# Kernel optimization log

Measured on AMD Instinct MI355X. Metric: run time of the kernel, lower is better.

Reference implementation:

```python
import jax, jax.numpy as jnp
import numpy as np
import math

B, N, M = 4, 2048, 2048
DIM_Q = DIM_K = DIM_V = 1024
H = 16

def setup_inputs() -> dict:
    key = jax.random.key(0)
    ks = jax.random.split(key, 10)
    s = 0.02
    return {
        "Q": jax.random.normal(ks[0], (B, N, DIM_Q), jnp.float32),
        "K": jax.random.normal(ks[1], (B, M, DIM_K), jnp.float32),
        "Wq": jax.random.normal(ks[2], (DIM_V, DIM_Q), jnp.float32) * s,
        "bq": jax.random.normal(ks[3], (DIM_V,), jnp.float32) * s,
        "Wk": jax.random.normal(ks[4], (DIM_V, DIM_K), jnp.float32) * s,
        "bk": jax.random.normal(ks[5], (DIM_V,), jnp.float32) * s,
        "Wv": jax.random.normal(ks[6], (DIM_V, DIM_K), jnp.float32) * s,
        "bv": jax.random.normal(ks[7], (DIM_V,), jnp.float32) * s,
        "Wo": jax.random.normal(ks[8], (DIM_V, DIM_V), jnp.float32) * s,
        "bo": jax.random.normal(ks[9], (DIM_V,), jnp.float32) * s,
    }

def reference(Q, K, Wq, bq, Wk, bk, Wv, bv, Wo, bo):
    d = DIM_V // H  # head dim
    Qp = Q @ Wq.T + bq            # [B,N,DIM_V]
    Kp = K @ Wk.T + bk            # [B,M,DIM_V]
    Vp = K @ Wv.T + bv            # [B,M,DIM_V]
    # split heads: [B,T,H,d] -> [B,H,T,d]
    Qh = Qp.reshape(B, N, H, d).transpose(0, 2, 1, 3)
    Kh = Kp.reshape(B, M, H, d).transpose(0, 2, 1, 3)
    Vh = Vp.reshape(B, M, H, d).transpose(0, 2, 1, 3)
    # NOTE: original scales by sqrt(dim_V), not sqrt(head_dim)
    scores = jnp.einsum('bhnd,bhmd->bhnm', Qh, Kh) / math.sqrt(DIM_V)
    A = jax.nn.softmax(scores, axis=-1)
    Oh = Qh + jnp.einsum('bhnm,bhmd->bhnd', A, Vh)   # residual with projected Q
    O = Oh.transpose(0, 2, 1, 3).reshape(B, N, DIM_V)
    O = O + jax.nn.relu(O @ Wo.T + bo)
    return O
```

## Files before the change

### kernel.cpp

```cpp
#include <hip/hip_runtime.h>
#include <cstddef>
#include <cstdint>


typedef unsigned short ushort_t;
typedef __attribute__((ext_vector_type(8))) short bf16x8;
typedef __attribute__((ext_vector_type(4))) float floatx4;
typedef __attribute__((ext_vector_type(2))) float f32x2;
typedef __attribute__((ext_vector_type(2))) __bf16 b16x2;
typedef __attribute__((ext_vector_type(4))) unsigned short us4;

__device__ __forceinline__ ushort_t f2bf(float x) {
  union { float f; unsigned u; } v; v.f = x;
  unsigned r = v.u + 0x7FFFu + ((v.u >> 16) & 1u);
  return (ushort_t)(r >> 16);
}
__device__ __forceinline__ float bf2f(ushort_t x) {
  union { unsigned u; float f; } v; v.u = ((unsigned)x) << 16;
  return v.f;
}
__device__ __forceinline__ unsigned pk2(float a, float b) {
  union { float f; unsigned u; } x, y; x.f = a; y.f = b;
  return __builtin_amdgcn_perm(y.u + 0x8000u, x.u + 0x8000u, 0x07060302u);
}
__device__ __forceinline__ unsigned pk2c(float a, float b) {
  union { b16x2 v; unsigned u; } r;
  r.v = __builtin_convertvector((f32x2){a, b}, b16x2);
  return r.u;
}
__device__ __forceinline__ floatx4 mfma16(bf16x8 a, bf16x8 b, floatx4 c) {
  return __builtin_amdgcn_mfma_f32_16x16x32_bf16(a, b, c, 0, 0, 0);
}
__device__ __forceinline__ void gld_lds16(const void* g, void* l) {
  __builtin_amdgcn_global_load_lds(
      (const __attribute__((address_space(1))) unsigned int*)g,
      (__attribute__((address_space(3))) unsigned int*)l, 16, 0, 0);
}

__global__ void cvt6(const float* __restrict__ i0, const float* __restrict__ i1,
                     const float* __restrict__ i2, const float* __restrict__ i3,
                     const float* __restrict__ i4, const float* __restrict__ i5,
                     ushort_t* __restrict__ o0, ushort_t* __restrict__ o1,
                     ushort_t* __restrict__ o2, ushort_t* __restrict__ o3,
                     ushort_t* __restrict__ o4, ushort_t* __restrict__ o5) {
  int z = blockIdx.z;
  const float* in = z == 0 ? i0 : z == 1 ? i1 : z == 2 ? i2 : z == 3 ? i3 : z == 4 ? i4 : i5;
  ushort_t* out = z == 0 ? o0 : z == 1 ? o1 : z == 2 ? o2 : z == 3 ? o3 : z == 4 ? o4 : o5;
  int n8 = (z < 2) ? 1048576 : 131072;
  int i = blockIdx.x * 256 + threadIdx.x;
  if (i < n8) {
    const float4* p = (const float4*)in + (size_t)i * 2;
    float4 a = p[0], b = p[1];
    uint4 o;
    o.x = pk2(a.x, a.y); o.y = pk2(a.z, a.w);
    o.z = pk2(b.x, b.y); o.w = pk2(b.z, b.w);
    *((uint4*)out + i) = o;
  }
}

__global__ __launch_bounds__(256, 2)
void gemm_qkv(const ushort_t* __restrict__ Qb, const ushort_t* __restrict__ Kb,
              const ushort_t* __restrict__ Wqb, const ushort_t* __restrict__ Wkb,
              const ushort_t* __restrict__ Wvb,
              const float* __restrict__ bq, const float* __restrict__ bk,
              const float* __restrict__ bv,
              ushort_t* __restrict__ Qp, ushort_t* __restrict__ Kp,
              ushort_t* __restrict__ Vt)
{
  const int Kd = 1024, Nn = 1024;
  const int z = blockIdx.z;
  const ushort_t* Ab = (z == 0) ? Qb : Kb;
  const ushort_t* Bw = (z == 0) ? Wqb : (z == 1) ? Wkb : Wvb;
  const float* bias  = (z == 0) ? bq : (z == 1) ? bk : bv;

  __shared__ __align__(16) ushort_t As[128][64];
  __shared__ __align__(16) ushort_t Bs[128][64];
  const int tid = threadIdx.x;
  const int lane = tid & 63, wave = tid >> 6;
  const int wm = (wave >> 1) * 64, wn = (wave & 1) * 64;
  const int rq = lane & 15, kg = lane >> 4;

  const int wg = blockIdx.x, xcd = wg & 7, slot = wg >> 3;
  const int by = xcd * 8 + (slot >> 3);
  const int bx = slot & 7;
  const int row0 = by * 128, col0 = bx * 128;

  const int st_sub = lane >> 3;
  const int st_cs  = (lane & 7) ^ st_sub;

  floatx4 acc[4][4];
#pragma unroll
  for (int i = 0; i < 4; ++i)
#pragma unroll
    for (int j = 0; j < 4; ++j) acc[i][j] = (floatx4){0.f, 0.f, 0.f, 0.f};

  for (int k0 = 0; k0 < Kd; k0 += 64) {
    __syncthreads();
#pragma unroll
    for (int r = 0; r < 4; ++r) {
      int i = wave * 4 + r;
      int row = i * 8 + st_sub;
      gld_lds16(Ab + (size_t)(row0 + row) * Kd + k0 + st_cs * 8, (ushort_t*)As + i * 512);
      gld_lds16(Bw + (size_t)(col0 + row) * Kd + k0 + st_cs * 8, (ushort_t*)Bs + i * 512);
    }
    __syncthreads();
#pragma unroll
    for (int kq = 0; kq < 2; ++kq) {
      bf16x8 af[4], bfr[4];
#pragma unroll
      for (int mi = 0; mi < 4; ++mi)
        af[mi] = *(const bf16x8*)&As[wm + mi*16 + rq][((kq*4 + kg) ^ (rq & 7)) * 8];
#pragma unroll
      for (int ni = 0; ni < 4; ++ni)
        bfr[ni] = *(const bf16x8*)&Bs[wn + ni*16 + rq][((kq*4 + kg) ^ (rq & 7)) * 8];
#pragma unroll
      for (int mi = 0; mi < 4; ++mi)
#pragma unroll
        for (int ni = 0; ni < 4; ++ni)
          acc[mi][ni] = mfma16(af[mi], bfr[ni], acc[mi][ni]);
    }
  }

  float bv4[4];
#pragma unroll
  for (int ni = 0; ni < 4; ++ni) bv4[ni] = bias[col0 + wn + ni*16 + rq];

  if (z < 2) {
    ushort_t* Cb = (z == 0) ? Qp : Kp;
#pragma unroll
    for (int mi = 0; mi < 4; ++mi)
#pragma unroll
      for (int ni = 0; ni < 4; ++ni)
#pragma unroll
        for (int rr = 0; rr < 4; ++rr) {
          int row = row0 + wm + mi*16 + kg*4 + rr;
          int col = col0 + wn + ni*16 + rq;
          Cb[(size_t)row * Nn + col] = f2bf(acc[mi][ni][rr] + bv4[ni]);
        }
  } else {
#pragma unroll
    for (int mi = 0; mi < 4; ++mi)
#pragma unroll
      for (int ni = 0; ni < 4; ++ni) {
        int col = col0 + wn + ni*16 + rq;
        int base32 = row0 + wm + (mi >> 1) * 32;
        int p = kg * 8 + (mi & 1) * 4;
        us4 o = { f2bf(acc[mi][ni][0] + bv4[ni]), f2bf(acc[mi][ni][1] + bv4[ni]),
                  f2bf(acc[mi][ni][2] + bv4[ni]), f2bf(acc[mi][ni][3] + bv4[ni]) };
        *(us4*)(Vt + (size_t)col * 8192 + base32 + p) = o;
      }
  }
}

__global__ __launch_bounds__(256, 2)
void gemm_out(const ushort_t* __restrict__ Ob, const ushort_t* __restrict__ Bw,
              const float* __restrict__ bias, float* __restrict__ Out)
{
  const int Kd = 1024, Nn = 1024;
  __shared__ __align__(16) ushort_t As[128][64];
  __shared__ __align__(16) ushort_t Bs[128][64];
  const int tid = threadIdx.x;
  const int lane = tid & 63, wave = tid >> 6;
  const int wm = (wave >> 1) * 64, wn = (wave & 1) * 64;
  const int rq = lane & 15, kg = lane >> 4;

  const int wg = blockIdx.x, xcd = wg & 7, slot = wg >> 3;
  const int by = xcd * 8 + (slot >> 3);
  const int bx = slot & 7;
  const int row0 = by * 128, col0 = bx * 128;

  const int st_sub = lane >> 3;
  const int st_cs  = (lane & 7) ^ st_sub;

  floatx4 acc[4][4];
#pragma unroll
  for (int i = 0; i < 4; ++i)
#pragma unroll
    for (int j = 0; j < 4; ++j) acc[i][j] = (floatx4){0.f, 0.f, 0.f, 0.f};

  for (int k0 = 0; k0 < Kd; k0 += 64) {
    __syncthreads();
#pragma unroll
    for (int r = 0; r < 4; ++r) {
      int i = wave * 4 + r;
      int row = i * 8 + st_sub;
      gld_lds16(Ob + (size_t)(row0 + row) * Kd + k0 + st_cs * 8, (ushort_t*)As + i * 512);
      gld_lds16(Bw + (size_t)(col0 + row) * Kd + k0 + st_cs * 8, (ushort_t*)Bs + i * 512);
    }
    __syncthreads();
#pragma unroll
    for (int kq = 0; kq < 2; ++kq) {
      bf16x8 af[4], bfr[4];
#pragma unroll
      for (int mi = 0; mi < 4; ++mi)
        af[mi] = *(const bf16x8*)&As[wm + mi*16 + rq][((kq*4 + kg) ^ (rq & 7)) * 8];
#pragma unroll
      for (int ni = 0; ni < 4; ++ni)
        bfr[ni] = *(const bf16x8*)&Bs[wn + ni*16 + rq][((kq*4 + kg) ^ (rq & 7)) * 8];
#pragma unroll
      for (int mi = 0; mi < 4; ++mi)
#pragma unroll
        for (int ni = 0; ni < 4; ++ni)
          acc[mi][ni] = mfma16(af[mi], bfr[ni], acc[mi][ni]);
    }
  }

  float bv4[4];
#pragma unroll
  for (int ni = 0; ni < 4; ++ni) bv4[ni] = bias[col0 + wn + ni*16 + rq];
#pragma unroll
  for (int mi = 0; mi < 4; ++mi)
#pragma unroll
    for (int ni = 0; ni < 4; ++ni)
#pragma unroll
      for (int rr = 0; rr < 4; ++rr) {
        int row = row0 + wm + mi*16 + kg*4 + rr;
        int col = col0 + wn + ni*16 + rq;
        size_t idx = (size_t)row * Nn + col;
        float pre = acc[mi][ni][rr] + bv4[ni];
        Out[idx] = bf2f(Ob[idx]) + (pre > 0.f ? pre : 0.f);
      }
}

__global__ __launch_bounds__(256, 2)
void attn_kernel(const ushort_t* __restrict__ Qp,
                 const ushort_t* __restrict__ Kp,
                 const ushort_t* __restrict__ Vt,
                 ushort_t* __restrict__ Ob)
{
  const float sc2 = 0.045084439f;
  const int wg = blockIdx.x, xcd = wg & 7, slot = wg >> 3;
  const int bh = xcd * 8 + (slot >> 4);
  const int qt = slot & 15;
  const int b = bh >> 4, h = bh & 15;
  const int q0 = qt * 128;

  __shared__ __align__(16) ushort_t Ks[2][8192];
  __shared__ __align__(16) ushort_t Vs[2][8192];

  const int tid = threadIdx.x, lane = tid & 63, wq = tid >> 6;
  const int rq = lane & 15, kg = lane >> 4;

  const size_t qkbase = (size_t)(b * 2048) * 1024 + h * 64;

  const int sg_sub = lane >> 3;
  const int sg_csk = (lane & 7) ^ sg_sub;

#pragma unroll
  for (int r = 0; r < 4; ++r) {
    int i = wq * 4 + r;
    int row = i * 8 + sg_sub;
    gld_lds16(Qp + qkbase + (size_t)(q0 + row) * 1024 + sg_csk * 8, &Ks[1][i * 512]);
  }
  __syncthreads();

  auto stage = [&](int kt, int bufi) {
    const int kv0 = kt * 128;
#pragma unroll
    for (int r = 0; r < 4; ++r) {
      int i = wq * 4 + r;
      int rowk = i * 8 + sg_sub;
      gld_lds16(Kp + qkbase + (size_t)(kv0 + rowk) * 1024 + sg_csk * 8,
                &Ks[bufi][i * 512]);
      int dv = i * 4 + (lane >> 4);
      int csv = (lane & 15) ^ (dv & 7);
      gld_lds16(Vt + (size_t)(h * 64 + dv) * 8192 + b * 2048 + kv0 + csv * 8,
                &Vs[bufi][i * 512]);
    }
  };
  stage(0, 0);

  bf16x8 aq[2][2];
#pragma unroll
  for (int ni = 0; ni < 2; ++ni)
#pragma unroll
    for (int kq = 0; kq < 2; ++kq) {
      int row = wq * 32 + ni * 16 + rq;
      int ch = (kq * 4 + kg) ^ (rq & 7);
      bf16x8 t = *(const bf16x8*)&Ks[1][row * 64 + ch * 8];
#pragma unroll
      for (int e = 0; e < 8; ++e)
        t[e] = (short)f2bf(bf2f((ushort_t)t[e]) * sc2);
      aq[ni][kq] = t;
    }

  bf16x8 ones;
#pragma unroll
  for (int e = 0; e < 8; ++e) ones[e] = (short)0x3F80;

  const floatx4 zf = (floatx4){0.f, 0.f, 0.f, 0.f};

  floatx4 oacc[2][4];
  floatx4 lacc[2];
#pragma unroll
  for (int nb = 0; nb < 2; ++nb) {
    lacc[nb] = (floatx4){0.f,0.f,0.f,0.f};
#pragma unroll
    for (int dvb = 0; dvb < 4; ++dvb) oacc[nb][dvb] = (floatx4){0.f,0.f,0.f,0.f};
  }

  __syncthreads();

  int cur = 0;
#pragma unroll 2
  for (int kt = 0; kt < 16; ++kt) {
    if (kt < 15) stage(kt + 1, cur ^ 1);

    floatx4 s[8][2];
    __builtin_amdgcn_s_setprio(1);
    {
      bf16x8 ak[8];
#pragma unroll
      for (int mi = 0; mi < 8; ++mi)
        ak[mi] = *(const bf16x8*)&Ks[cur][(mi * 16 + rq) * 64 + ((kg ^ (rq & 7)) * 8)];
#pragma unroll
      for (int mi = 0; mi < 8; ++mi)
#pragma unroll
        for (int ni = 0; ni < 2; ++ni)
          s[mi][ni] = mfma16(ak[mi], aq[ni][0], zf);
#pragma unroll
      for (int mi = 0; mi < 8; ++mi)
        ak[mi] = *(const bf16x8*)&Ks[cur][(mi * 16 + rq) * 64 + (((4 + kg) ^ (rq & 7)) * 8)];
#pragma unroll
      for (int mi = 0; mi < 8; ++mi)
#pragma unroll
        for (int ni = 0; ni < 2; ++ni)
          s[mi][ni] = mfma16(ak[mi], aq[ni][1], s[mi][ni]);
    }
    __builtin_amdgcn_s_setprio(0);

#pragma unroll
    for (int mi = 0; mi < 2; ++mi)
#pragma unroll
      for (int ni = 0; ni < 2; ++ni)
#pragma unroll
        for (int rr = 0; rr < 4; ++rr)
          s[mi][ni][rr] = __builtin_amdgcn_exp2f(s[mi][ni][rr]);

#pragma unroll
    for (int c = 0; c < 4; ++c) {
      bf16x8 vf[4];
#pragma unroll
      for (int dvb = 0; dvb < 4; ++dvb) {
        int dv = dvb * 16 + rq;
        int ch = (c * 4 + kg) ^ (rq & 7);
        vf[dvb] = *(const bf16x8*)&Vs[cur][dv * 128 + ch * 8];
      }
      union { unsigned u[4]; bf16x8 v; } pa0, pa1;
      pa0.u[0] = pk2c(s[2*c  ][0][0], s[2*c  ][0][1]);
      pa0.u[1] = pk2c(s[2*c  ][0][2], s[2*c  ][0][3]);
      pa0.u[2] = pk2c(s[2*c+1][0][0], s[2*c+1][0][1]);
      pa0.u[3] = pk2c(s[2*c+1][0][2], s[2*c+1][0][3]);
      pa1.u[0] = pk2c(s[2*c  ][1][0], s[2*c  ][1][1]);
      pa1.u[1] = pk2c(s[2*c  ][1][2], s[2*c  ][1][3]);
      pa1.u[2] = pk2c(s[2*c+1][1][0], s[2*c+1][1][1]);
      pa1.u[3] = pk2c(s[2*c+1][1][2], s[2*c+1][1][3]);
      __builtin_amdgcn_s_setprio(1);
#pragma unroll
      for (int dvb = 0; dvb < 4; ++dvb) {
        oacc[0][dvb] = mfma16(pa0.v, vf[dvb], oacc[0][dvb]);
        oacc[1][dvb] = mfma16(pa1.v, vf[dvb], oacc[1][dvb]);
      }
      lacc[0] = mfma16(pa0.v, ones, lacc[0]);
      lacc[1] = mfma16(pa1.v, ones, lacc[1]);
      __builtin_amdgcn_s_setprio(0);
      if (c < 3) {
#pragma unroll
        for (int mi = 2*c + 2; mi < 2*c + 4; ++mi)
#pragma unroll
          for (int ni = 0; ni < 2; ++ni)
#pragma unroll
            for (int rr = 0; rr < 4; ++rr)
              s[mi][ni][rr] = __builtin_amdgcn_exp2f(s[mi][ni][rr]);
      }
    }

    __syncthreads();
    cur ^= 1;
  }

#pragma unroll
  for (int nb = 0; nb < 2; ++nb)
#pragma unroll
    for (int rr = 0; rr < 4; ++rr) {
      int row = wq * 32 + nb * 16 + kg * 4 + rr;
      float linv = 1.0f / lacc[nb][rr];
#pragma unroll
      for (int dvb = 0; dvb < 4; ++dvb) {
        int col = dvb * 16 + rq;
        size_t idx = qkbase + (size_t)(q0 + row) * 1024 + col;
        Ob[idx] = f2bf(oacc[nb][dvb][rr] * linv + bf2f(Qp[idx]));
      }
    }
}

extern "C" void kernel_launch(void* const* d_in, const int* in_sizes, int n_in,
                              void* d_out, int out_size, void* d_ws, size_t ws_size,
                              hipStream_t stream)
{
  const float* Q  = (const float*)d_in[0];
  const float* K  = (const float*)d_in[1];
  const float* Wq = (const float*)d_in[2];
  const float* bq = (const float*)d_in[3];
  const float* Wk = (const float*)d_in[4];
  const float* bk = (const float*)d_in[5];
  const float* Wv = (const float*)d_in[6];
  const float* bv = (const float*)d_in[7];
  const float* Wo = (const float*)d_in[8];
  const float* bo = (const float*)d_in[9];
  float* Out = (float*)d_out;

  ushort_t* ws = (ushort_t*)d_ws;
  const size_t E = (size_t)8192 * 1024;
  const size_t WSZ = (size_t)1024 * 1024;
  ushort_t* Qb  = ws;
  ushort_t* Kb  = ws + E;
  ushort_t* Qp  = ws + 2*E;
  ushort_t* Kp  = ws + 3*E;
  ushort_t* Vt  = ws + 4*E;
  ushort_t* Wqb = ws + 5*E;
  ushort_t* Wkb = ws + 5*E + WSZ;
  ushort_t* Wvb = ws + 5*E + 2*WSZ;
  ushort_t* Wob = ws + 5*E + 3*WSZ;
  ushort_t* Ob  = Qb;

  cvt6<<<dim3(4096, 1, 6), 256, 0, stream>>>(Q, K, Wq, Wk, Wv, Wo,
                                             Qb, Kb, Wqb, Wkb, Wvb, Wob);

  dim3 blk(256);
  gemm_qkv<<<dim3(512, 1, 3), blk, 0, stream>>>(Qb, Kb, Wqb, Wkb, Wvb,
                                                bq, bk, bv, Qp, Kp, Vt);
  attn_kernel<<<dim3(1024), blk, 0, stream>>>(Qp, Kp, Vt, Ob);
  gemm_out<<<dim3(512), blk, 0, stream>>>(Ob, Wob, bo, Out);
}
```

Measured before the change: 285.0 us.

## Pre-swizzle V into fragment order and load directly to registers, bypassing LDS

The V projection epilogue now writes V in a per-(batch,head,tile) layout matching the MFMA B-fragment order. The attention kernel then loads V fragments straight from global memory into registers with coalesced 16-byte loads, dropping the V LDS buffers and their staging. This halves LDS use and removes LDS reads for V, but it puts global-load latency in the loop, relying on L2 and on issuing the loads early, and it raises register pressure with 16 extra vector fragments.

```diff
diff --git a/kernel.cpp b/kernel.cpp
--- a/kernel.cpp
+++ b/kernel.cpp
@@ -143,11 +143,15 @@
 #pragma unroll
       for (int ni = 0; ni < 4; ++ni) {
         int col = col0 + wn + ni*16 + rq;
-        int base32 = row0 + wm + (mi >> 1) * 32;
-        int p = kg * 8 + (mi & 1) * 4;
+        int h = col >> 6, dvb = (col >> 4) & 3;
+        int kvg = row0 + wm + (mi >> 1) * 32;
+        int bI = kvg >> 11, kv = kvg & 2047;
+        int t = kv >> 7, c = (kv >> 5) & 3;
+        size_t addr = (size_t)(bI * 16 + h) * 131072 + t * 8192
+                    + (c * 4 + dvb) * 512 + (kg * 16 + rq) * 8 + (mi & 1) * 4;
         us4 o = { f2bf(acc[mi][ni][0] + bv4[ni]), f2bf(acc[mi][ni][1] + bv4[ni]),
                   f2bf(acc[mi][ni][2] + bv4[ni]), f2bf(acc[mi][ni][3] + bv4[ni]) };
-        *(us4*)(Vt + (size_t)col * 8192 + base32 + p) = o;
+        *(us4*)(Vt + addr) = o;
       }
   }
 }
@@ -236,12 +240,12 @@
   const int q0 = qt * 128;
 
   __shared__ __align__(16) ushort_t Ks[2][8192];
-  __shared__ __align__(16) ushort_t Vs[2][8192];
 
   const int tid = threadIdx.x, lane = tid & 63, wq = tid >> 6;
   const int rq = lane & 15, kg = lane >> 4;
 
   const size_t qkbase = (size_t)(b * 2048) * 1024 + h * 64;
+  const ushort_t* vbase = Vt + (size_t)bh * 131072 + lane * 8;
 
   const int sg_sub = lane >> 3;
   const int sg_csk = (lane & 7) ^ sg_sub;
@@ -262,10 +266,6 @@
       int rowk = i * 8 + sg_sub;
       gld_lds16(Kp + qkbase + (size_t)(kv0 + rowk) * 1024 + sg_csk * 8,
                 &Ks[bufi][i * 512]);
-      int dv = i * 4 + (lane >> 4);
-      int csv = (lane & 15) ^ (dv & 7);
-      gld_lds16(Vt + (size_t)(h * 64 + dv) * 8192 + b * 2048 + kv0 + csv * 8,
-                &Vs[bufi][i * 512]);
     }
   };
   stage(0, 0);
@@ -304,6 +304,13 @@
   int cur = 0;
 #pragma unroll 2
   for (int kt = 0; kt < 16; ++kt) {
+    const ushort_t* vtile = vbase + kt * 8192;
+
+    bf16x8 vfa[16];
+#pragma unroll
+    for (int j = 0; j < 8; ++j)
+      vfa[j] = *(const bf16x8*)(vtile + j * 512);
+
     if (kt < 15) stage(kt + 1, cur ^ 1);
 
     floatx4 s[8][2];
@@ -330,6 +337,10 @@
     __builtin_amdgcn_s_setprio(0);
 
 #pragma unroll
+    for (int j = 8; j < 16; ++j)
+      vfa[j] = *(const bf16x8*)(vtile + j * 512);
+
+#pragma unroll
     for (int mi = 0; mi < 2; ++mi)
 #pragma unroll
       for (int ni = 0; ni < 2; ++ni)
@@ -339,13 +350,6 @@
 
 #pragma unroll
     for (int c = 0; c < 4; ++c) {
-      bf16x8 vf[4];
-#pragma unroll
-      for (int dvb = 0; dvb < 4; ++dvb) {
-        int dv = dvb * 16 + rq;
-        int ch = (c * 4 + kg) ^ (rq & 7);
-        vf[dvb] = *(const bf16x8*)&Vs[cur][dv * 128 + ch * 8];
-      }
       union { unsigned u[4]; bf16x8 v; } pa0, pa1;
       pa0.u[0] = pk2c(s[2*c  ][0][0], s[2*c  ][0][1]);
       pa0.u[1] = pk2c(s[2*c  ][0][2], s[2*c  ][0][3]);
@@ -358,8 +362,8 @@
       __builtin_amdgcn_s_setprio(1);
 #pragma unroll
       for (int dvb = 0; dvb < 4; ++dvb) {
-        oacc[0][dvb] = mfma16(pa0.v, vf[dvb], oacc[0][dvb]);
-        oacc[1][dvb] = mfma16(pa1.v, vf[dvb], oacc[1][dvb]);
+        oacc[0][dvb] = mfma16(pa0.v, vfa[c*4+dvb], oacc[0][dvb]);
+        oacc[1][dvb] = mfma16(pa1.v, vfa[c*4+dvb], oacc[1][dvb]);
       }
       lacc[0] = mfma16(pa0.v, ones, lacc[0]);
       lacc[1] = mfma16(pa1.v, ones, lacc[1]);
```

After: 298.7 us. 4.8% more time.
